# Performance work log

Hardware: AMD Instinct MI355X
Metric: run time of the kernel (lower is better)

The kernel has to match this reference:

```python
import jax, jax.numpy as jnp
import numpy as np

EPS = 1e-5  # torch BatchNorm1d default eps
NH, KD, D_V = 8, 64, 128  # num_heads, key_dim, per-head value dim (attn_ratio*key_dim)


def hardswish(x):
    return x * jnp.clip(x + 3.0, 0.0, 6.0) / 6.0


def linear_bn(x, W, g, b):
    # Linear (no bias) followed by BatchNorm1d in training mode: batch stats
    # over all leading dims (torch flattens (B,N) before BN).
    y = x @ W.T
    yf = y.reshape(-1, y.shape[-1])
    mu = yf.mean(0)
    var = yf.var(0)  # biased variance, matching BN normalization
    return (y - mu) * (g / jnp.sqrt(var + EPS)) + b


def setup_inputs() -> dict:
    key = jax.random.key(0)
    ks = jax.random.split(key, 22)
    B, C, H, W, NT, D = 8, 1024, 96, 96, 60, 512
    dh = NH * D_V          # 1024
    h_kv = dh + NH * KD    # 1536
    hf = 2 * D             # 1024 (mr=2)

    def p(k, shape, s=0.02):
        return jax.random.normal(k, shape, jnp.float32) * s

    return {
        "im_emd": jax.random.normal(ks[0], (B, C, H, W), jnp.float32),
        "text_emd": jax.random.normal(ks[1], (NT, D), jnp.float32),
        "W_dc": p(ks[2], (D, C)), "g_dc": 1.0 + p(ks[3], (D,)), "b_dc": p(ks[4], (D,)),
        "W_kv": p(ks[5], (h_kv, D)), "g_kv": 1.0 + p(ks[6], (h_kv,)), "b_kv": p(ks[7], (h_kv,)),
        "W_q": p(ks[8], (NH * KD, D)), "g_q": 1.0 + p(ks[9], (NH * KD,)), "b_q": p(ks[10], (NH * KD,)),
        "W_proj": p(ks[11], (D, dh)), "g_proj": 1.0 + p(ks[12], (D,)), "b_proj": p(ks[13], (D,)),
        "biases": p(ks[14], (NH, 10000)),  # relative-position bias table (100x100 offsets)
        "W_f1": p(ks[15], (hf, D)), "g_f1": 1.0 + p(ks[16], (hf,)), "b_f1": p(ks[17], (hf,)),
        "W_f2": p(ks[18], (D, hf)), "g_f2": 1.0 + p(ks[19], (D,)), "b_f2": p(ks[20], (D,)),
    }


def _bias_idx(NT, H, W):
    # Offset table built row-major over product(range(100), range(100)) =>
    # attention_offsets[(a,b)] == 100*a + b. Text token t maps to grid point
    # (t//100, t%100); image token n to (n//W, n%W).
    t = np.arange(NT)
    n = np.arange(H * W)
    dx = np.abs(t[:, None] // 100 - n[None, :] // W)
    dy = np.abs(t[:, None] % 100 - n[None, :] % W)
    return 100 * dx + dy  # [NT, N]


def reference(im_emd, text_emd, W_dc, g_dc, b_dc, W_kv, g_kv, b_kv,
              W_q, g_q, b_q, W_proj, g_proj, b_proj, biases,
              W_f1, g_f1, b_f1, W_f2, g_f2, b_f2):
    B, C, H, W = im_emd.shape
    N = H * W
    NT, D = text_emd.shape
    dh = NH * D_V
    scale = KD ** -0.5

    # image tokens -> embed_dim
    x = im_emd.reshape(B, C, N).transpose(0, 2, 1)          # [B,N,C]
    xd = hardswish(linear_bn(x, W_dc, g_dc, b_dc))          # [B,N,D]

    # Attentioninv: text queries attend over image keys/values
    kv = linear_bn(xd, W_kv, g_kv, b_kv).reshape(B, N, NH, KD + D_V)
    k, v = kv[..., :KD], kv[..., KD:]                       # [B,N,h,64], [B,N,h,128]
    q = linear_bn(text_emd[None], W_q, g_q, b_q).reshape(NT, NH, KD)  # [NT,h,64]

    idx = jnp.asarray(_bias_idx(NT, H, W))                  # [NT,N] static
    bias = biases[:, idx]                                   # [h,NT,N] gather

    attn = jnp.einsum('thd,bnhd->bhtn', q, k) * scale + bias[None]
    attn = jax.nn.softmax(attn, axis=-1)                    # [B,h,NT,N]
    out = jnp.einsum('bhtn,bnhd->bthd', attn, v).reshape(B, NT, dh)
    out = linear_bn(hardswish(out), W_proj, g_proj, b_proj)  # [B,NT,D]

    textd = text_emd[None] + out                            # residual (broadcast)

    # ffntext: Linear_BN -> Hardswish -> Linear_BN(bn_weight_init=0) + residual
    f = hardswish(linear_bn(textd, W_f1, g_f1, b_f1))
    f = linear_bn(f, W_f2, g_f2, b_f2)
    textd = f + textd
    return textd[0]  # [NT, D]
```

## Files before the change

kernel.cpp:

```cpp
#include <hip/hip_runtime.h>
#include <hip/hip_bf16.h>
#include <stdint.h>

typedef short bf16x8 __attribute__((ext_vector_type(8)));
typedef float f32x4 __attribute__((ext_vector_type(4)));

__device__ __forceinline__ float b2f(ushort u){ return __uint_as_float(((uint32_t)u)<<16); }
__device__ __forceinline__ ushort f2b(float f){
  uint32_t u = __float_as_uint(f);
  u += 0x7fffu + ((u>>16)&1u);
  return (ushort)(u>>16);
}
__device__ __forceinline__ float hswish(float x){ return x*fminf(fmaxf(x+3.f,0.f),6.f)*(1.f/6.f); }

__device__ __forceinline__ void gll16(const void* g, void* l){
  __builtin_amdgcn_global_load_lds((const __attribute__((address_space(1))) void*)g,
                                   (__attribute__((address_space(3))) void*)l, 16, 0, 0);
}

__global__ void init_kernel(const float* __restrict__ Wdc, const float* __restrict__ Wkv,
                            ushort* __restrict__ Wdc_b, ushort* __restrict__ Wkv_b,
                            float* __restrict__ zbase){
  int i = blockIdx.x*256 + threadIdx.x;
  if (i < 8192) zbase[i] = 0.f;
  for (int j=i; j<512*1024; j+=262144) Wdc_b[j] = f2b(Wdc[j]);
  for (int j=i; j<1536*512; j+=262144) Wkv_b[j] = f2b(Wkv[j]);
}

__global__ __launch_bounds__(256) void transpose_kernel(const float* __restrict__ im, ushort* __restrict__ At){
  __shared__ float tb[64][65];
  const int b = blockIdx.z, c0 = blockIdx.y*64, n0 = blockIdx.x*64;
  const int tid = threadIdx.x;
  const int cl = tid >> 2, q = tid & 3;
  #pragma unroll
  for (int it=0; it<4; ++it){
    int nn = q*4 + it*16;
    float4 v = *(const float4*)&im[((size_t)(b*1024 + c0 + cl))*9216 + n0 + nn];
    tb[cl][nn+0]=v.x; tb[cl][nn+1]=v.y; tb[cl][nn+2]=v.z; tb[cl][nn+3]=v.w;
  }
  __syncthreads();
  const int nr = tid >> 4, c4 = (tid & 15)*4;
  #pragma unroll
  for (int ps=0; ps<4; ++ps){
    int nn = nr + ps*16;
    ushort4 u;
    u.x = f2b(tb[c4+0][nn]); u.y = f2b(tb[c4+1][nn]);
    u.z = f2b(tb[c4+2][nn]); u.w = f2b(tb[c4+3][nn]);
    *(ushort4*)&At[((size_t)(b*9216 + n0 + nn))*1024 + c0 + c4] = u;
  }
}

template<int SPLIT>
__global__ __launch_bounds__(256) void gemm_bt(
    const ushort* __restrict__ A, const ushort* __restrict__ Bm,
    ushort* __restrict__ Cm, ushort* __restrict__ Vt,
    float* __restrict__ sums, float* __restrict__ sqs,
    int NT, int N, int K)
{
  __shared__ __align__(16) ushort As[128*64];
  __shared__ __align__(16) ushort Bs[128*64];
  const int tid = threadIdx.x;
  const int l = tid & 63;
  const int w = tid >> 6;
  const int wm = w >> 1, wn = w & 1;
  const int chunk = gridDim.x >> 3;
  const int wg = (blockIdx.x & 7)*chunk + (blockIdx.x >> 3);
  const int tn = wg % NT, tm = wg / NT;
  const size_t n0 = (size_t)tn * 128;
  const size_t m0 = (size_t)tm * 128;
  const int lr = l & 15, lk = l >> 4;
  const int wbase = tid & ~63;

  f32x4 acc[4][4];
  #pragma unroll
  for (int i=0;i<4;++i)
    #pragma unroll
    for (int j=0;j<4;++j) acc[i][j] = (f32x4){0.f,0.f,0.f,0.f};

  for (int kt = 0; kt < K; kt += 64) {
    #pragma unroll
    for (int it=0; it<4; ++it) {
      int idx = it*256 + tid;
      int row = idx >> 3, c8 = idx & 7;
      int sc8 = c8 ^ (row & 7);
      gll16(&A[(m0+row)*K + kt + sc8*8], &As[(it*256 + wbase)*8]);
      gll16(&Bm[(n0+row)*K + kt + sc8*8], &Bs[(it*256 + wbase)*8]);
    }
    __syncthreads();
    #pragma unroll
    for (int kk=0; kk<64; kk+=32) {
      bf16x8 af[4], bfr[4];
      #pragma unroll
      for (int i=0;i<4;++i){
        int row = wm*64 + i*16 + lr;
        af[i] = *(const bf16x8*)&As[row*64 + ((kk + lk*8) ^ ((row&7)<<3))];
      }
      #pragma unroll
      for (int j=0;j<4;++j){
        int row = wn*64 + j*16 + lr;
        bfr[j] = *(const bf16x8*)&Bs[row*64 + ((kk + lk*8) ^ ((row&7)<<3))];
      }
      #pragma unroll
      for (int i=0;i<4;++i)
        #pragma unroll
        for (int j=0;j<4;++j)
          acc[i][j] = __builtin_amdgcn_mfma_f32_16x16x32_bf16(af[i], bfr[j], acc[i][j], 0, 0, 0);
    }
    __syncthreads();
  }
  if constexpr (SPLIT==0){
    #pragma unroll
    for (int i=0;i<4;++i)
      #pragma unroll
      for (int j=0;j<4;++j)
        #pragma unroll
        for (int r=0;r<4;++r) {
          size_t row = m0 + wm*64 + i*16 + lk*4 + r;
          size_t col = n0 + wn*64 + j*16 + lr;
          Cm[row*N + col] = f2b(acc[i][j][r]);
        }
  } else {
    const int bq = (int)(m0/9216);
    const int nbase = (int)(m0 - (size_t)bq*9216);
    #pragma unroll
    for (int j=0;j<4;++j){
      int c = (int)n0 + wn*64 + j*16 + lr;
      int h = c/192, rcol = c - h*192;
      #pragma unroll
      for (int i=0;i<4;++i){
        int nrow = nbase + wm*64 + i*16 + lk*4;
        if (rcol < 64){
          ushort* kb = Cm + ((size_t)(bq*9216 + nrow))*512 + h*64 + rcol;
          #pragma unroll
          for (int r=0;r<4;++r) kb[(size_t)r*512] = f2b(acc[i][j][r]);
        } else {
          int dv = rcol - 64;
          ushort4 u;
          u.x=f2b(acc[i][j][0]); u.y=f2b(acc[i][j][1]);
          u.z=f2b(acc[i][j][2]); u.w=f2b(acc[i][j][3]);
          *(ushort4*)&Vt[((size_t)((bq*8+h)*128 + dv))*9216 + nrow] = u;
        }
      }
    }
  }
  #pragma unroll
  for (int j=0;j<4;++j){
    float cs=0.f, cq=0.f;
    #pragma unroll
    for (int i=0;i<4;++i)
      #pragma unroll
      for (int r=0;r<4;++r){ float v=acc[i][j][r]; cs+=v; cq+=v*v; }
    cs += __shfl_xor(cs,16); cs += __shfl_xor(cs,32);
    cq += __shfl_xor(cq,16); cq += __shfl_xor(cq,32);
    if (lk==0){
      int col = (int)n0 + wn*64 + j*16 + lr;
      atomicAdd(&sums[col], cs);
      atomicAdd(&sqs [col], cq);
    }
  }
}

__global__ __launch_bounds__(256) void bn_hswish(ushort* __restrict__ y,
    const float* __restrict__ ssum, const float* __restrict__ ssq,
    const float* __restrict__ g, const float* __restrict__ bb)
{
  __shared__ float sc[512], sh[512];
  const float invn = 1.f/73728.f;
  for (int i=threadIdx.x;i<512;i+=256){
    float mu = ssum[i]*invn;
    float var = ssq[i]*invn - mu*mu;
    float k = g[i]*rsqrtf(var+1e-5f);
    sc[i]=k; sh[i]=bb[i]-mu*k;
  }
  __syncthreads();
  const size_t total = (size_t)73728*512/8;
  for (size_t idx = (size_t)blockIdx.x*256+threadIdx.x; idx < total; idx += (size_t)gridDim.x*256){
    uint4 u = *(uint4*)&y[idx*8];
    ushort* up = (ushort*)&u;
    int c0 = ((int)(idx & 63))*8;
    #pragma unroll
    for (int e=0;e<8;++e){
      float x = b2f(up[e])*sc[c0+e] + sh[c0+e];
      up[e] = f2b(hswish(x));
    }
    *(uint4*)&y[idx*8] = u;
  }
}

__global__ __launch_bounds__(256) void q_gemm(const float* __restrict__ text, const float* __restrict__ Wq, float* __restrict__ qraw)
{
  __shared__ __align__(16) float xr[512];
  const int t = blockIdx.x, tid = threadIdx.x;
  for (int i=tid;i<512;i+=256) xr[i] = text[t*512+i];
  __syncthreads();
  #pragma unroll
  for (int cj=0;cj<2;++cj){
    int c = cj*256+tid;
    const float4* wp = (const float4*)(Wq + (size_t)c*512);
    const float4* xp = (const float4*)xr;
    float a=0.f;
    for (int u=0;u<128;++u){
      float4 wv = wp[u], xv = xp[u];
      a += wv.x*xv.x + wv.y*xv.y + wv.z*xv.z + wv.w*xv.w;
    }
    qraw[t*512+c]=a;
  }
}

__global__ __launch_bounds__(512) void q_bn_qh(const float* __restrict__ qraw,
                                               const float* __restrict__ g, const float* __restrict__ bb,
                                               const float* __restrict__ s2sum, const float* __restrict__ s2sq,
                                               const float* __restrict__ g_kv, const float* __restrict__ b_kv,
                                               ushort* __restrict__ Qh, float* __restrict__ cQ)
{
  const int c = threadIdx.x;
  const int h = c >> 6, d = c & 63;
  float s=0.f,q=0.f;
  for (int t=0;t<60;++t){ float v = qraw[t*512+c]; s+=v; q+=v*v; }
  float mu=s*(1.f/60.f), var=q*(1.f/60.f)-mu*mu;
  float k = g[c]*rsqrtf(var+1e-5f);
  float sh = bb[c]-mu*k;
  const float invn = 1.f/73728.f;
  float mu2 = s2sum[h*192+d]*invn;
  float var2 = s2sq[h*192+d]*invn - mu2*mu2;
  float k2 = g_kv[h*192+d]*rsqrtf(var2+1e-5f);
  const float sk = k2*0.125f;
  const float tk = (b_kv[h*192+d]-mu2*k2)*0.125f;
  for (int t=0;t<60;++t){
    float qv = qraw[t*512+c]*k+sh;
    Qh[(h*64+t)*64+d] = f2b(qv*sk);
    float contrib = qv*tk;
    #pragma unroll
    for (int o=32;o>0;o>>=1) contrib += __shfl_xor(contrib,o);
    if (d==0) cQ[h*64+t] = contrib;
  }
  for (int t=60;t<64;++t) Qh[(h*64+t)*64+d] = 0;
  if (d==0) for (int t=60;t<64;++t) cQ[h*64+t] = 0.f;
}

__global__ __launch_bounds__(256) void attn_flash(
    const ushort* __restrict__ Qh, const float* __restrict__ cQ,
    const ushort* __restrict__ Kbuf, const ushort* __restrict__ Vt,
    const float* __restrict__ biases,
    float* __restrict__ Op, float* __restrict__ Mp, float* __restrict__ Lp)
{
  __shared__ __align__(16) ushort Qs[64*72];
  __shared__ __align__(16) ushort vt[128*64];
  __shared__ __align__(16) ushort Pw[4][16*72];
  __shared__ float bias_l[2400];
  __shared__ float cQs[64];
  const int tid = threadIdx.x;
  const int l = tid & 63, w = tid >> 6;
  const int lr = l & 15, lk = l >> 4;
  const int nc = blockIdx.x, h = blockIdx.y, b = blockIdx.z;
  const int bh = b*8+h;
  const int wbase = tid & ~63;
  for (int cid = tid; cid < 512; cid += 256){
    int row = cid >> 3, c8 = cid & 7;
    *(uint4*)&Qs[row*72 + c8*8] = *(const uint4*)&Qh[(size_t)(h*64+row)*64 + c8*8];
  }
  for (int i = tid; i < 2400; i += 256) bias_l[i] = biases[h*10000 + nc*2400 + i];
  if (tid < 64) cQs[tid] = cQ[h*64 + tid];

  const ushort* vsrc = Vt + (size_t)bh*128*9216;
  const ushort* kchunk = Kbuf + (size_t)b*9216*512 + h*64;

  float m_run[4] = {-1e30f,-1e30f,-1e30f,-1e30f};
  float l_run[4] = {0.f,0.f,0.f,0.f};
  f32x4 acc_o[8];
  #pragma unroll
  for (int j=0;j<8;++j) acc_o[j] = (f32x4){0.f,0.f,0.f,0.f};
  __syncthreads();

  for (int tile=0; tile<36; ++tile){
    const int n0 = nc*2304 + tile*64;
    if (tile) __syncthreads();
    #pragma unroll
    for (int it=0; it<4; ++it){
      int idx = it*256 + tid;
      int row = idx >> 3, c8 = idx & 7;
      int sc8 = c8 ^ (row & 7);
      gll16(&vsrc[(size_t)row*9216 + n0 + sc8*8], &vt[(it*256 + wbase)*8]);
    }
    __syncthreads();
    f32x4 sa[4];
    #pragma unroll
    for (int j=0;j<4;++j) sa[j]=(f32x4){0.f,0.f,0.f,0.f};
    const ushort* kbase = kchunk + (size_t)n0*512;
    __builtin_amdgcn_s_setprio(1);
    #pragma unroll
    for (int kk=0; kk<64; kk+=32){
      bf16x8 af = *(const bf16x8*)&Qs[(w*16+lr)*72 + kk + lk*8];
      #pragma unroll
      for (int j=0;j<4;++j){
        bf16x8 bf_ = *(const bf16x8*)&kbase[(size_t)(j*16+lr)*512 + kk + lk*8];
        sa[j] = __builtin_amdgcn_mfma_f32_16x16x32_bf16(af, bf_, sa[j], 0,0,0);
      }
    }
    __builtin_amdgcn_s_setprio(0);
    float mt[4] = {-1e30f,-1e30f,-1e30f,-1e30f};
    #pragma unroll
    for (int j=0;j<4;++j){
      int n = n0 + j*16 + lr;
      int py = n/96;
      int px = n - py*96;
      int pyl = py - nc*24;
      #pragma unroll
      for (int r=0;r<4;++r){
        int t = w*16 + lk*4 + r;
        int dd = t - px; dd = dd<0?-dd:dd;
        float s = sa[j][r] + cQs[t] + bias_l[pyl*100 + dd];
        sa[j][r] = s;
        mt[r] = fmaxf(mt[r], s);
      }
    }
    #pragma unroll
    for (int r=0;r<4;++r){
      #pragma unroll
      for (int o=1;o<16;o<<=1) mt[r] = fmaxf(mt[r], __shfl_xor(mt[r], o));
      float mnew = fmaxf(m_run[r], mt[r]);
      float ef = __expf(m_run[r] - mnew);
      m_run[r] = mnew;
      l_run[r] *= ef;
      #pragma unroll
      for (int j2=0;j2<8;++j2) acc_o[j2][r] *= ef;
    }
    float rs[4] = {0.f,0.f,0.f,0.f};
    #pragma unroll
    for (int j=0;j<4;++j)
      #pragma unroll
      for (int r=0;r<4;++r){
        float pe = __expf(sa[j][r] - m_run[r]);
        rs[r] += pe;
        Pw[w][(lk*4+r)*72 + j*16 + lr] = f2b(pe);
      }
    #pragma unroll
    for (int r=0;r<4;++r){
      #pragma unroll
      for (int o=1;o<16;o<<=1) rs[r] += __shfl_xor(rs[r], o);
      l_run[r] += rs[r];
    }
    __builtin_amdgcn_s_setprio(1);
    #pragma unroll
    for (int kk=0; kk<64; kk+=32){
      bf16x8 pa = *(const bf16x8*)&Pw[w][lr*72 + kk + lk*8];
      #pragma unroll
      for (int j2=0;j2<8;++j2){
        int dv = j2*16 + lr;
        bf16x8 vb = *(const bf16x8*)&vt[dv*64 + ((kk + lk*8) ^ ((dv&7)<<3))];
        acc_o[j2] = __builtin_amdgcn_mfma_f32_16x16x32_bf16(pa, vb, acc_o[j2], 0,0,0);
      }
    }
    __builtin_amdgcn_s_setprio(0);
  }
  float* ob = Op + (((size_t)nc*64 + bh)*64)*128;
  #pragma unroll
  for (int j2=0;j2<8;++j2)
    #pragma unroll
    for (int r=0;r<4;++r){
      int row = w*16 + lk*4 + r;
      ob[(size_t)row*128 + j2*16 + lr] = acc_o[j2][r];
    }
  if (lr == 0){
    #pragma unroll
    for (int r=0;r<4;++r){
      int row = w*16 + lk*4 + r;
      Mp[(nc*64+bh)*64 + row] = m_run[r];
      Lp[(nc*64+bh)*64 + row] = l_run[r];
    }
  }
}

__global__ __launch_bounds__(128) void attn_combine(
    const float* __restrict__ Op, const float* __restrict__ Mp, const float* __restrict__ Lp,
    float* __restrict__ attn_o)
{
  const int t = blockIdx.x, bh = blockIdx.y;
  const int b = bh >> 3, h = bh & 7;
  const int dv = threadIdx.x;
  float mv[4];
  float m_g = -1e30f;
  #pragma unroll
  for (int i=0;i<4;++i){ mv[i] = Mp[(i*64+bh)*64 + t]; m_g = fmaxf(m_g, mv[i]); }
  float lsum = 0.f;
  #pragma unroll
  for (int i=0;i<4;++i) lsum += Lp[(i*64+bh)*64 + t] * __expf(mv[i]-m_g);
  float o = 0.f;
  #pragma unroll
  for (int i=0;i<4;++i)
    o += Op[(((size_t)i*64 + bh)*64 + t)*128 + dv] * __expf(mv[i]-m_g);
  attn_o[(size_t)(b*60+t)*1024 + h*128 + dv] = o / lsum;
}

template<int CIN, int COUT, int MODE>
__global__ __launch_bounds__(256) void rowgemm8(
    const float* __restrict__ X, const float* __restrict__ Wt,
    const float* __restrict__ isum, const float* __restrict__ isq,
    const float* __restrict__ ig, const float* __restrict__ ib, float invn,
    const float* __restrict__ text, float* __restrict__ textd,
    float* __restrict__ out, float* __restrict__ osum, float* __restrict__ osq)
{
  __shared__ __align__(16) float xr[8][CIN];
  __shared__ float scf[CIN], shf[CIN];
  const int rb0 = blockIdx.x*8, tid = threadIdx.x;
  for (int i=tid; i<CIN; i+=256){
    int idx = (MODE==3) ? (64 + (i&127) + (i>>7)*192) : i;
    float mu = isum[idx]*invn;
    float var = isq[idx]*invn - mu*mu;
    float k = ig[idx]*rsqrtf(var+1e-5f);
    scf[i]=k; shf[i]=ib[idx]-mu*k;
  }
  __syncthreads();
  for (int i=tid; i<8*CIN; i+=256){
    int rr = i / CIN, cc = i % CIN;
    float v = X[(size_t)(rb0+rr)*CIN + cc];
    v = v*scf[cc] + shf[cc];
    if constexpr (MODE==2 || MODE==3) v = hswish(v);
    if constexpr (MODE==4){
      int t = (rb0+rr) % 60;
      v = text[t*CIN+cc] + v;
      if (blockIdx.y == 0) textd[(size_t)(rb0+rr)*CIN + cc] = v;
    }
    xr[rr][cc]=v;
  }
  __syncthreads();
  int c = blockIdx.y*256 + tid;
  const float4* wp = (const float4*)(Wt + (size_t)c*CIN);
  float a[8] = {0.f,0.f,0.f,0.f,0.f,0.f,0.f,0.f};
  for (int u=0;u<CIN/4;++u){
    float4 wv = wp[u];
    #pragma unroll
    for (int rr=0;rr<8;++rr){
      float4 xv = *(const float4*)&xr[rr][u*4];
      a[rr] += wv.x*xv.x + wv.y*xv.y + wv.z*xv.z + wv.w*xv.w;
    }
  }
  float ps=0.f, pq=0.f;
  #pragma unroll
  for (int rr=0;rr<8;++rr){
    out[(size_t)(rb0+rr)*COUT + c] = a[rr];
    ps += a[rr]; pq += a[rr]*a[rr];
  }
  atomicAdd(&osum[c], ps);
  atomicAdd(&osq [c], pq);
}

__global__ void final_out(const float* __restrict__ f2raw,
                          const float* __restrict__ ssum, const float* __restrict__ ssq,
                          const float* __restrict__ g, const float* __restrict__ bb,
                          const float* __restrict__ textd, float* __restrict__ outp)
{
  int i = blockIdx.x*256+threadIdx.x;
  if (i < 60*512){
    int c = i & 511;
    float mu = ssum[c]*(1.f/480.f);
    float var = ssq[c]*(1.f/480.f) - mu*mu;
    float k = g[c]*rsqrtf(var+1e-5f);
    outp[i] = f2raw[i]*k + (bb[c]-mu*k) + textd[i];
  }
}

extern "C" void kernel_launch(void* const* d_in, const int* in_sizes, int n_in,
                              void* d_out, int out_size, void* d_ws, size_t ws_size,
                              hipStream_t stream)
{
  (void)in_sizes; (void)n_in; (void)out_size; (void)ws_size;
  const float* im    = (const float*)d_in[0];
  const float* text  = (const float*)d_in[1];
  const float* W_dc  = (const float*)d_in[2];
  const float* g_dc  = (const float*)d_in[3];
  const float* b_dc  = (const float*)d_in[4];
  const float* W_kv  = (const float*)d_in[5];
  const float* g_kv  = (const float*)d_in[6];
  const float* b_kv  = (const float*)d_in[7];
  const float* W_q   = (const float*)d_in[8];
  const float* g_q   = (const float*)d_in[9];
  const float* b_q   = (const float*)d_in[10];
  const float* W_proj= (const float*)d_in[11];
  const float* g_proj= (const float*)d_in[12];
  const float* b_proj= (const float*)d_in[13];
  const float* biases= (const float*)d_in[14];
  const float* W_f1  = (const float*)d_in[15];
  const float* g_f1  = (const float*)d_in[16];
  const float* b_f1  = (const float*)d_in[17];
  const float* W_f2  = (const float*)d_in[18];
  const float* g_f2  = (const float*)d_in[19];
  const float* b_f2  = (const float*)d_in[20];
  float* outp = (float*)d_out;

  char* p = (char*)d_ws;
  auto alloc = [&](size_t bytes)->char*{ char* r = p; p += (bytes+255)&~(size_t)255; return r; };
  float* s1_sum = (float*)alloc(512*4);
  float* s1_sq  = (float*)alloc(512*4);
  float* s2_sum = (float*)alloc(1536*4);
  float* s2_sq  = (float*)alloc(1536*4);
  float* s3_sum = (float*)alloc(512*4);
  float* s3_sq  = (float*)alloc(512*4);
  float* s4_sum = (float*)alloc(1024*4);
  float* s4_sq  = (float*)alloc(1024*4);
  float* s5_sum = (float*)alloc(512*4);
  float* s5_sq  = (float*)alloc(512*4);
  float* zero_base = s1_sum;
  float* attn_o = (float*)alloc((size_t)480*1024*4);
  float* qraw = (float*)alloc(60*512*4);
  ushort* Qh = (ushort*)alloc((size_t)8*64*64*2);
  float* cQ = (float*)alloc(512*4);
  float* proj_raw = (float*)alloc((size_t)480*512*4);
  float* textd=(float*)alloc((size_t)480*512*4);
  float* f1_raw=(float*)alloc((size_t)480*1024*4);
  float* f2_raw=(float*)alloc((size_t)480*512*4);
  float* Op = (float*)alloc((size_t)4*64*64*128*4);
  float* Mp = (float*)alloc((size_t)4*64*64*4);
  float* Lp = (float*)alloc((size_t)4*64*64*4);
  ushort* Wdc_b = (ushort*)alloc((size_t)512*1024*2);
  ushort* Wkv_b = (ushort*)alloc((size_t)1536*512*2);
  ushort* y1 = (ushort*)alloc((size_t)73728*512*2);
  ushort* Kbuf = (ushort*)alloc((size_t)73728*512*2);
  ushort* Vt  = (ushort*)alloc((size_t)64*128*9216*2);
  ushort* At = (ushort*)alloc((size_t)73728*1024*2);

  init_kernel<<<1024,256,0,stream>>>(W_dc, W_kv, Wdc_b, Wkv_b, zero_base);
  transpose_kernel<<<dim3(144,16,8),256,0,stream>>>(im, At);
  gemm_bt<0><<<2304,256,0,stream>>>(At, Wdc_b, y1, nullptr, s1_sum, s1_sq, 4, 512, 1024);
  bn_hswish<<<2048,256,0,stream>>>(y1, s1_sum, s1_sq, g_dc, b_dc);
  gemm_bt<1><<<6912,256,0,stream>>>(y1, Wkv_b, Kbuf, Vt, s2_sum, s2_sq, 12, 1536, 512);
  q_gemm<<<60,256,0,stream>>>(text, W_q, qraw);
  q_bn_qh<<<1,512,0,stream>>>(qraw, g_q, b_q, s2_sum, s2_sq, g_kv, b_kv, Qh, cQ);
  attn_flash<<<dim3(4,8,8),256,0,stream>>>(Qh, cQ, Kbuf, Vt, biases, Op, Mp, Lp);
  attn_combine<<<dim3(60,64),128,0,stream>>>(Op, Mp, Lp, attn_o);
  rowgemm8<1024,512,3><<<dim3(60,2),256,0,stream>>>(attn_o, W_proj, s2_sum, s2_sq, g_kv, b_kv, 1.f/73728.f,
                                                    nullptr, nullptr, proj_raw, s3_sum, s3_sq);
  rowgemm8<512,1024,4><<<dim3(60,4),256,0,stream>>>(proj_raw, W_f1, s3_sum, s3_sq, g_proj, b_proj, 1.f/480.f,
                                                    text, textd, f1_raw, s4_sum, s4_sq);
  rowgemm8<1024,512,2><<<dim3(60,2),256,0,stream>>>(f1_raw, W_f2, s4_sum, s4_sq, g_f1, b_f1, 1.f/480.f,
                                                    nullptr, nullptr, f2_raw, s5_sum, s5_sq);
  final_out<<<120,256,0,stream>>>(f2_raw, s5_sum, s5_sq, g_f2, b_f2, textd, outp);
}
```

Measured before the change: 755.3 us.

## Fuse image transpose into first GEMM and split attention over more chunks

Result: no change. 751.2 us (-0.5%).

```diff
diff --git a/kernel.cpp b/kernel.cpp
--- a/kernel.cpp
+++ b/kernel.cpp
@@ -27,30 +27,108 @@
   for (int j=i; j<1536*512; j+=262144) Wkv_b[j] = f2b(Wkv[j]);
 }
 
-__global__ __launch_bounds__(256) void transpose_kernel(const float* __restrict__ im, ushort* __restrict__ At){
-  __shared__ float tb[64][65];
-  const int b = blockIdx.z, c0 = blockIdx.y*64, n0 = blockIdx.x*64;
+__global__ __launch_bounds__(256) void gemm_im(
+    const float* __restrict__ im, const ushort* __restrict__ Bm,
+    ushort* __restrict__ Cm, float* __restrict__ sums, float* __restrict__ sqs)
+{
+  __shared__ __align__(16) float Tf[64*128];
+  __shared__ __align__(16) ushort As[128*64];
+  __shared__ __align__(16) ushort Bs[128*64];
   const int tid = threadIdx.x;
-  const int cl = tid >> 2, q = tid & 3;
-  #pragma unroll
-  for (int it=0; it<4; ++it){
-    int nn = q*4 + it*16;
-    float4 v = *(const float4*)&im[((size_t)(b*1024 + c0 + cl))*9216 + n0 + nn];
-    tb[cl][nn+0]=v.x; tb[cl][nn+1]=v.y; tb[cl][nn+2]=v.z; tb[cl][nn+3]=v.w;
-  }
-  __syncthreads();
-  const int nr = tid >> 4, c4 = (tid & 15)*4;
-  #pragma unroll
-  for (int ps=0; ps<4; ++ps){
-    int nn = nr + ps*16;
-    ushort4 u;
-    u.x = f2b(tb[c4+0][nn]); u.y = f2b(tb[c4+1][nn]);
-    u.z = f2b(tb[c4+2][nn]); u.w = f2b(tb[c4+3][nn]);
-    *(ushort4*)&At[((size_t)(b*9216 + n0 + nn))*1024 + c0 + c4] = u;
-  }
-}
-
-template<int SPLIT>
+  const int l = tid & 63;
+  const int w = tid >> 6;
+  const int wm = w >> 1, wn = w & 1;
+  const int chunk = gridDim.x >> 3;
+  const int wg = (blockIdx.x & 7)*chunk + (blockIdx.x >> 3);
+  const int tn = wg % 4, tm = wg / 4;
+  const size_t n0 = (size_t)tn * 128;
+  const int bq = tm / 72;
+  const int p0 = (tm - bq*72) * 128;
+  const int lr = l & 15, lk = l >> 4;
+  const int wbase = tid & ~63;
+
+  f32x4 acc[4][4];
+  #pragma unroll
+  for (int i=0;i<4;++i)
+    #pragma unroll
+    for (int j=0;j<4;++j) acc[i][j] = (f32x4){0.f,0.f,0.f,0.f};
+
+  for (int kt = 0; kt < 1024; kt += 64) {
+    #pragma unroll
+    for (int it=0; it<4; ++it) {
+      int idx = it*256 + tid;
+      int row = idx >> 3, c8 = idx & 7;
+      int sc8 = c8 ^ (row & 7);
+      gll16(&Bm[(n0+row)*1024 + kt + sc8*8], &Bs[(it*256 + wbase)*8]);
+    }
+    const float* imb = im + ((size_t)(bq*1024 + kt))*9216 + p0;
+    #pragma unroll
+    for (int it=0; it<8; ++it){
+      int task = it*256 + tid;
+      int c = task >> 5, g = task & 31;
+      float4 v = *(const float4*)&imb[(size_t)c*9216 + g*4];
+      *(float4*)&Tf[c*128 + g*4] = v;
+    }
+    __syncthreads();
+    #pragma unroll
+    for (int it=0; it<4; ++it){
+      int task = it*256 + tid;
+      int p = task & 127, grp = task >> 7;
+      ushort tmp[8];
+      #pragma unroll
+      for (int e=0;e<8;++e) tmp[e] = f2b(Tf[(grp*8+e)*128 + p]);
+      *(uint4*)&As[p*64 + ((grp ^ (p&7))<<3)] = *(const uint4*)tmp;
+    }
+    __syncthreads();
+    #pragma unroll
+    for (int kk=0; kk<64; kk+=32) {
+      bf16x8 af[4], bfr[4];
+      #pragma unroll
+      for (int i=0;i<4;++i){
+        int row = wm*64 + i*16 + lr;
+        af[i] = *(const bf16x8*)&As[row*64 + ((kk + lk*8) ^ ((row&7)<<3))];
+      }
+      #pragma unroll
+      for (int j=0;j<4;++j){
+        int row = wn*64 + j*16 + lr;
+        bfr[j] = *(const bf16x8*)&Bs[row*64 + ((kk + lk*8) ^ ((row&7)<<3))];
+      }
+      #pragma unroll
+      for (int i=0;i<4;++i)
+        #pragma unroll
+        for (int j=0;j<4;++j)
+          acc[i][j] = __builtin_amdgcn_mfma_f32_16x16x32_bf16(af[i], bfr[j], acc[i][j], 0, 0, 0);
+    }
+    __syncthreads();
+  }
+  const size_t m0 = (size_t)bq*9216 + p0;
+  #pragma unroll
+  for (int i=0;i<4;++i)
+    #pragma unroll
+    for (int j=0;j<4;++j)
+      #pragma unroll
+      for (int r=0;r<4;++r) {
+        size_t row = m0 + wm*64 + i*16 + lk*4 + r;
+        size_t col = n0 + wn*64 + j*16 + lr;
+        Cm[row*512 + col] = f2b(acc[i][j][r]);
+      }
+  #pragma unroll
+  for (int j=0;j<4;++j){
+    float cs=0.f, cq=0.f;
+    #pragma unroll
+    for (int i=0;i<4;++i)
+      #pragma unroll
+      for (int r=0;r<4;++r){ float v=acc[i][j][r]; cs+=v; cq+=v*v; }
+    cs += __shfl_xor(cs,16); cs += __shfl_xor(cs,32);
+    cq += __shfl_xor(cq,16); cq += __shfl_xor(cq,32);
+    if (lk==0){
+      int col = (int)n0 + wn*64 + j*16 + lr;
+      atomicAdd(&sums[col], cs);
+      atomicAdd(&sqs [col], cq);
+    }
+  }
+}
+
 __global__ __launch_bounds__(256) void gemm_bt(
     const ushort* __restrict__ A, const ushort* __restrict__ Bm,
     ushort* __restrict__ Cm, ushort* __restrict__ Vt,
@@ -108,18 +186,7 @@
     }
     __syncthreads();
   }
-  if constexpr (SPLIT==0){
-    #pragma unroll
-    for (int i=0;i<4;++i)
-      #pragma unroll
-      for (int j=0;j<4;++j)
-        #pragma unroll
-        for (int r=0;r<4;++r) {
-          size_t row = m0 + wm*64 + i*16 + lk*4 + r;
-          size_t col = n0 + wn*64 + j*16 + lr;
-          Cm[row*N + col] = f2b(acc[i][j][r]);
-        }
-  } else {
+  {
     const int bq = (int)(m0/9216);
     const int nbase = (int)(m0 - (size_t)bq*9216);
     #pragma unroll
@@ -247,7 +314,7 @@
   __shared__ __align__(16) ushort Qs[64*72];
   __shared__ __align__(16) ushort vt[128*64];
   __shared__ __align__(16) ushort Pw[4][16*72];
-  __shared__ float bias_l[2400];
+  __shared__ float bias_l[600];
   __shared__ float cQs[64];
   const int tid = threadIdx.x;
   const int l = tid & 63, w = tid >> 6;
@@ -259,7 +326,7 @@
     int row = cid >> 3, c8 = cid & 7;
     *(uint4*)&Qs[row*72 + c8*8] = *(const uint4*)&Qh[(size_t)(h*64+row)*64 + c8*8];
   }
-  for (int i = tid; i < 2400; i += 256) bias_l[i] = biases[h*10000 + nc*2400 + i];
+  for (int i = tid; i < 600; i += 256) bias_l[i] = biases[h*10000 + nc*600 + i];
   if (tid < 64) cQs[tid] = cQ[h*64 + tid];
 
   const ushort* vsrc = Vt + (size_t)bh*128*9216;
@@ -272,8 +339,8 @@
   for (int j=0;j<8;++j) acc_o[j] = (f32x4){0.f,0.f,0.f,0.f};
   __syncthreads();
 
-  for (int tile=0; tile<36; ++tile){
-    const int n0 = nc*2304 + tile*64;
+  for (int tile=0; tile<9; ++tile){
+    const int n0 = nc*576 + tile*64;
     if (tile) __syncthreads();
     #pragma unroll
     for (int it=0; it<4; ++it){
@@ -304,7 +371,7 @@
       int n = n0 + j*16 + lr;
       int py = n/96;
       int px = n - py*96;
-      int pyl = py - nc*24;
+      int pyl = py - nc*6;
       #pragma unroll
       for (int r=0;r<4;++r){
         int t = w*16 + lk*4 + r;
@@ -378,16 +445,16 @@
   const int t = blockIdx.x, bh = blockIdx.y;
   const int b = bh >> 3, h = bh & 7;
   const int dv = threadIdx.x;
-  float mv[4];
+  float mv[16];
   float m_g = -1e30f;
   #pragma unroll
-  for (int i=0;i<4;++i){ mv[i] = Mp[(i*64+bh)*64 + t]; m_g = fmaxf(m_g, mv[i]); }
+  for (int i=0;i<16;++i){ mv[i] = Mp[(i*64+bh)*64 + t]; m_g = fmaxf(m_g, mv[i]); }
   float lsum = 0.f;
   #pragma unroll
-  for (int i=0;i<4;++i) lsum += Lp[(i*64+bh)*64 + t] * __expf(mv[i]-m_g);
+  for (int i=0;i<16;++i) lsum += Lp[(i*64+bh)*64 + t] * __expf(mv[i]-m_g);
   float o = 0.f;
   #pragma unroll
-  for (int i=0;i<4;++i)
+  for (int i=0;i<16;++i)
     o += Op[(((size_t)i*64 + bh)*64 + t)*128 + dv] * __expf(mv[i]-m_g);
   attn_o[(size_t)(b*60+t)*1024 + h*128 + dv] = o / lsum;
 }
@@ -509,24 +576,22 @@
   float* textd=(float*)alloc((size_t)480*512*4);
   float* f1_raw=(float*)alloc((size_t)480*1024*4);
   float* f2_raw=(float*)alloc((size_t)480*512*4);
-  float* Op = (float*)alloc((size_t)4*64*64*128*4);
-  float* Mp = (float*)alloc((size_t)4*64*64*4);
-  float* Lp = (float*)alloc((size_t)4*64*64*4);
+  float* Op = (float*)alloc((size_t)16*64*64*128*4);
+  float* Mp = (float*)alloc((size_t)16*64*64*4);
+  float* Lp = (float*)alloc((size_t)16*64*64*4);
   ushort* Wdc_b = (ushort*)alloc((size_t)512*1024*2);
   ushort* Wkv_b = (ushort*)alloc((size_t)1536*512*2);
   ushort* y1 = (ushort*)alloc((size_t)73728*512*2);
   ushort* Kbuf = (ushort*)alloc((size_t)73728*512*2);
   ushort* Vt  = (ushort*)alloc((size_t)64*128*9216*2);
-  ushort* At = (ushort*)alloc((size_t)73728*1024*2);
 
   init_kernel<<<1024,256,0,stream>>>(W_dc, W_kv, Wdc_b, Wkv_b, zero_base);
-  transpose_kernel<<<dim3(144,16,8),256,0,stream>>>(im, At);
-  gemm_bt<0><<<2304,256,0,stream>>>(At, Wdc_b, y1, nullptr, s1_sum, s1_sq, 4, 512, 1024);
+  gemm_im<<<2304,256,0,stream>>>(im, Wdc_b, y1, s1_sum, s1_sq);
   bn_hswish<<<2048,256,0,stream>>>(y1, s1_sum, s1_sq, g_dc, b_dc);
-  gemm_bt<1><<<6912,256,0,stream>>>(y1, Wkv_b, Kbuf, Vt, s2_sum, s2_sq, 12, 1536, 512);
+  gemm_bt<<<6912,256,0,stream>>>(y1, Wkv_b, Kbuf, Vt, s2_sum, s2_sq, 12, 1536, 512);
   q_gemm<<<60,256,0,stream>>>(text, W_q, qraw);
   q_bn_qh<<<1,512,0,stream>>>(qraw, g_q, b_q, s2_sum, s2_sq, g_kv, b_kv, Qh, cQ);
-  attn_flash<<<dim3(4,8,8),256,0,stream>>>(Qh, cQ, Kbuf, Vt, biases, Op, Mp, Lp);
+  attn_flash<<<dim3(16,8,8),256,0,stream>>>(Qh, cQ, Kbuf, Vt, biases, Op, Mp, Lp);
   attn_combine<<<dim3(60,64),128,0,stream>>>(Op, Mp, Lp, attn_o);
   rowgemm8<1024,512,3><<<dim3(60,2),256,0,stream>>>(attn_o, W_proj, s2_sum, s2_sq, g_kv, b_kv, 1.f/73728.f,
                                                     nullptr, nullptr, proj_raw, s3_sum, s3_sq);
```
